# Performance work log

Hardware: AMD Instinct MI355X
Metric: run time of the kernel (lower is better)

## Reference

```python
import jax, jax.numpy as jnp
import numpy as np

B, S = 128, 32
V, E, H, L = 32000, 512, 1024, 2


def setup_inputs() -> dict:
    key = jax.random.key(0)
    ks = jax.random.split(key, 16)
    s = 0.02  # weight scale
    inp = {
        "x": jax.random.randint(ks[0], (B, S), 0, V),
        "encoder_output": jax.random.normal(ks[1], (S, B, H), jnp.float32),  # unused by module
        "encoder_hidden_state": jax.random.normal(ks[2], (L, B, H), jnp.float32),
        "emb": jax.random.normal(ks[3], (V, E), jnp.float32) * s,
        "w_ih0": jax.random.normal(ks[4], (3 * H, E), jnp.float32) * s,
        "w_hh0": jax.random.normal(ks[5], (3 * H, H), jnp.float32) * s,
        "b_ih0": jax.random.normal(ks[6], (3 * H,), jnp.float32) * s,
        "b_hh0": jax.random.normal(ks[7], (3 * H,), jnp.float32) * s,
        "w_ih1": jax.random.normal(ks[8], (3 * H, H), jnp.float32) * s,
        "w_hh1": jax.random.normal(ks[9], (3 * H, H), jnp.float32) * s,
        "b_ih1": jax.random.normal(ks[10], (3 * H,), jnp.float32) * s,
        "b_hh1": jax.random.normal(ks[11], (3 * H,), jnp.float32) * s,
        "w_dec": jax.random.normal(ks[12], (V, H), jnp.float32) * s,
        "b_dec": jax.random.normal(ks[13], (V,), jnp.float32) * s,
        "max_seq_length": S,
    }
    return inp


def _gru_cell(h, xt, w_ih, w_hh, b_ih, b_hh):
    # PyTorch GRU gate math
    gi = xt @ w_ih.T + b_ih  # [B, 3H]
    gh = h @ w_hh.T + b_hh   # [B, 3H]
    ir, iz, inn = jnp.split(gi, 3, axis=-1)
    hr, hz, hn = jnp.split(gh, 3, axis=-1)
    r = jax.nn.sigmoid(ir + hr)
    z = jax.nn.sigmoid(iz + hz)
    n = jnp.tanh(inn + r * hn)
    return (1.0 - z) * n + z * h


def reference(x, encoder_output, encoder_hidden_state, emb,
              w_ih0, w_hh0, b_ih0, b_hh0,
              w_ih1, w_hh1, b_ih1, b_hh1,
              w_dec, b_dec, max_seq_length):
    # teaching_rate = 0.0 -> pure teacher forcing; dropout p=0.0 -> identity.
    # Step 0 consumes SOS token (id 1, from torch.ones().long()); steps 1..T-1 consume x[:, i].
    Bsz = x.shape[0]
    sos = jnp.ones((Bsz, 1), jnp.int32)
    toks = jnp.concatenate([sos, x[:, 1:max_seq_length].astype(jnp.int32)], axis=1)  # [B, T]
    xs = emb[toks].transpose(1, 0, 2)  # [T, B, E] (seq-first, matching permute(1,0,2))

    def step(carry, xt):
        h0, h1 = carry
        h0 = _gru_cell(h0, xt, w_ih0, w_hh0, b_ih0, b_hh0)
        h1 = _gru_cell(h1, h0, w_ih1, w_hh1, b_ih1, b_hh1)
        return (h0, h1), h1

    init = (encoder_hidden_state[0], encoder_hidden_state[1])
    _, ys = jax.lax.scan(step, init, xs)  # ys: [T, B, H]
    logits = jnp.einsum('tbh,vh->tbv', ys, w_dec) + b_dec  # [T, B, V]
    return logits
```

## Files before the change

kernel.cpp:

```cpp
#include <hip/hip_runtime.h>
#include <hip/hip_bf16.h>
#include <stdint.h>

#define T_SEQ 32
#define BATCH 128
#define EMB   512
#define HID   1024
#define VOC   32000
#define G3    (3 * HID)
#define MROWS (T_SEQ * BATCH)
#define BHID  (BATCH * HID)

typedef __bf16 bf16_t;
typedef __bf16 bf16x8 __attribute__((ext_vector_type(8)));
typedef __bf16 bf16x4 __attribute__((ext_vector_type(4)));
typedef float  f32x4  __attribute__((ext_vector_type(4)));

#define MFMA(a, b, c) __builtin_amdgcn_mfma_f32_16x16x32_bf16((a), (b), (c), 0, 0, 0)

__global__ void f32_to_bf16_kernel(const float* __restrict__ in,
                                   bf16_t* __restrict__ out, int n) {
    int i = (blockIdx.x * blockDim.x + threadIdx.x) * 4;
    if (i + 3 < n) {
        float4 v = *(const float4*)(in + i);
        out[i + 0] = (bf16_t)v.x;
        out[i + 1] = (bf16_t)v.y;
        out[i + 2] = (bf16_t)v.z;
        out[i + 3] = (bf16_t)v.w;
    } else {
        for (; i < n; ++i) out[i] = (bf16_t)in[i];
    }
}

__global__ void embed_kernel(const int* __restrict__ x,
                             const float* __restrict__ emb,
                             bf16_t* __restrict__ X) {
    int m = blockIdx.x;
    int t = m >> 7, b = m & 127;
    int tok = (t == 0) ? 1 : x[b * T_SEQ + t];
    const float* src = emb + (size_t)tok * EMB;
    bf16_t* dst = X + (size_t)m * EMB;
    int c = threadIdx.x * 4;
    float4 v = *(const float4*)(src + c);
    dst[c + 0] = (bf16_t)v.x;
    dst[c + 1] = (bf16_t)v.y;
    dst[c + 2] = (bf16_t)v.z;
    dst[c + 3] = (bf16_t)v.w;
}

#define GLOAD_LDS16(g, l)                                                    \
    __builtin_amdgcn_global_load_lds(                                        \
        (const __attribute__((address_space(1))) void*)(g),                  \
        (__attribute__((address_space(3))) void*)(l), 16, 0, 0)

template <int BIAS>
__global__ __launch_bounds__(256) void gemm_bf16_kernel(
    const bf16_t* __restrict__ A, const bf16_t* __restrict__ B,
    const float* __restrict__ bias, float* __restrict__ C,
    int M, int N, int K) {
    __shared__ __align__(16) bf16_t As[128 * 32];
    __shared__ __align__(16) bf16_t Bs[128 * 32];

    const int nbm = gridDim.y, nbn = gridDim.x;
    const int nwg = nbm * nbn;
    int lin = blockIdx.y * nbn + blockIdx.x;
    if ((nwg & 7) == 0) {
        int xcd = lin & 7, idx = lin >> 3;
        lin = xcd * (nwg >> 3) + idx;
    }
    const int bm = (lin % nbm) * 128;
    const int bn = (lin / nbm) * 128;

    const int tid  = threadIdx.x;
    const int lane = tid & 63;
    const int w    = tid >> 6;
    const int wr   = w >> 1, wc = w & 1;

    f32x4 acc[4][4] = {};

    const int lrow = tid >> 2;
    const int lcol = (tid & 3) * 8;
    const bf16_t* ag = A + (size_t)(bm + lrow) * K + lcol;
    const bf16_t* bg = B + (size_t)(bn + lrow) * K + lcol;
    bf16_t* asl0 = As + lrow * 32 + lcol;
    bf16_t* asl1 = As + (lrow + 64) * 32 + lcol;
    bf16_t* bsl0 = Bs + lrow * 32 + lcol;
    bf16_t* bsl1 = Bs + (lrow + 64) * 32 + lcol;

    const int r16 = lane & 15;
    const int kh  = (lane >> 4) * 8;

    for (int k0 = 0; k0 < K; k0 += 32) {
        GLOAD_LDS16(ag + k0, asl0);
        GLOAD_LDS16(ag + (size_t)64 * K + k0, asl1);
        GLOAD_LDS16(bg + k0, bsl0);
        GLOAD_LDS16(bg + (size_t)64 * K + k0, bsl1);
        __syncthreads();

        bf16x8 af[4], bf[4];
#pragma unroll
        for (int mi = 0; mi < 4; ++mi)
            af[mi] = *(const bf16x8*)(As + (wr * 64 + mi * 16 + r16) * 32 + kh);
#pragma unroll
        for (int ni = 0; ni < 4; ++ni)
            bf[ni] = *(const bf16x8*)(Bs + (wc * 64 + ni * 16 + r16) * 32 + kh);
#pragma unroll
        for (int mi = 0; mi < 4; ++mi)
#pragma unroll
            for (int ni = 0; ni < 4; ++ni)
                acc[mi][ni] = MFMA(af[mi], bf[ni], acc[mi][ni]);
        __syncthreads();
    }

#pragma unroll
    for (int mi = 0; mi < 4; ++mi) {
        const int row0 = bm + wr * 64 + mi * 16 + (lane >> 4) * 4;
#pragma unroll
        for (int ni = 0; ni < 4; ++ni) {
            const int col = bn + wc * 64 + ni * 16 + r16;
            float bv = 0.f;
            if (BIAS) bv = bias[col];
#pragma unroll
            for (int r = 0; r < 4; ++r)
                C[(size_t)(row0 + r) * N + col] = acc[mi][ni][r] + bv;
        }
    }
}

template <int BIAS>
__global__ __launch_bounds__(512, 1) void gemm256_bf16_kernel(
    const bf16_t* __restrict__ A, const bf16_t* __restrict__ B,
    const float* __restrict__ bias, float* __restrict__ C,
    int M, int N, int K) {
    __shared__ __align__(16) bf16_t lds[2 * 2 * 16384];

    const int NT = K >> 6;
    const int nbm = gridDim.y, nbn = gridDim.x;
    const int nwg = nbm * nbn;
    int lin = blockIdx.y * nbn + blockIdx.x;
    {
        int q = nwg >> 3, r = nwg & 7, x = lin & 7, i = lin >> 3;
        lin = (x < r ? x * (q + 1) : r * (q + 1) + (x - r) * q) + i;
    }
    const int bm = (lin % nbm) * 256;
    const int bn = (lin / nbm) * 256;

    const int tid = threadIdx.x, lane = tid & 63;
    const int w = tid >> 6, wm = w >> 2, wn = w & 3;
    const int r16 = lane & 15, sl = lane >> 4, r7 = r16 & 7;

    const int srow  = tid >> 3;
    const int sslot = (tid & 7) ^ (srow & 7);
    const bf16_t* agS = A + (size_t)(bm + srow) * K + sslot * 8;
    const bf16_t* bgS = B + (size_t)(bn + srow) * K + sslot * 8;

    const int colk0 = ((0 + sl) ^ r7) * 8;
    const int colk1 = ((4 + sl) ^ r7) * 8;
    const int arow = (wm * 128 + r16) * 64;
    const int brow = (wn * 64 + r16) * 64;

    f32x4 acc[8][4] = {};
    bf16x8 af[4][2], bf[4][2];

#pragma unroll
    for (int l = 0; l < 4; ++l)
        GLOAD_LDS16(agS + (size_t)(l * 64) * K, lds + l * 4096 + tid * 8);
#pragma unroll
    for (int l = 0; l < 4; ++l)
        GLOAD_LDS16(bgS + (size_t)(l * 64) * K, lds + 16384 + l * 4096 + tid * 8);
#pragma unroll
    for (int l = 0; l < 4; ++l)
        GLOAD_LDS16(agS + (size_t)(l * 64) * K + 64,
                    lds + 32768 + l * 4096 + tid * 8);
#pragma unroll
    for (int l = 0; l < 4; ++l)
        GLOAD_LDS16(bgS + (size_t)(l * 64) * K + 64,
                    lds + 49152 + l * 4096 + tid * 8);
    asm volatile("s_waitcnt vmcnt(8)" ::: "memory");
    __builtin_amdgcn_sched_barrier(0);
    __builtin_amdgcn_s_barrier();

#pragma unroll 1
    for (int kt = 0; kt < NT; ++kt) {
        const int cur = kt & 1;
        const bf16_t* Ab = lds + cur * 32768;
        const bf16_t* Bb = Ab + 16384;
        bf16_t* Sb = lds + cur * 32768;
        const bool st = (kt + 2 < NT);
        const size_t kof = (size_t)(kt + 2) * 64;

#pragma unroll
        for (int fr = 0; fr < 4; ++fr) {
            af[fr][0] = *(const bf16x8*)(Ab + arow + fr * 1024 + colk0);
            af[fr][1] = *(const bf16x8*)(Ab + arow + fr * 1024 + colk1);
        }
#pragma unroll
        for (int nf = 0; nf < 2; ++nf) {
            bf[nf][0] = *(const bf16x8*)(Bb + brow + nf * 1024 + colk0);
            bf[nf][1] = *(const bf16x8*)(Bb + brow + nf * 1024 + colk1);
        }
        __builtin_amdgcn_sched_barrier(0);
        __builtin_amdgcn_s_barrier();
        asm volatile("s_waitcnt lgkmcnt(0)" ::: "memory");
        __builtin_amdgcn_sched_barrier(0);
        __builtin_amdgcn_s_setprio(1);
#pragma unroll
        for (int fr = 0; fr < 4; ++fr)
#pragma unroll
            for (int nf = 0; nf < 2; ++nf) {
                acc[fr][nf] = MFMA(af[fr][0], bf[nf][0], acc[fr][nf]);
                acc[fr][nf] = MFMA(af[fr][1], bf[nf][1], acc[fr][nf]);
            }
        __builtin_amdgcn_s_setprio(0);
        __builtin_amdgcn_sched_barrier(0);
        __builtin_amdgcn_s_barrier();

#pragma unroll
        for (int nf = 2; nf < 4; ++nf) {
            bf[nf][0] = *(const bf16x8*)(Bb + brow + nf * 1024 + colk0);
            bf[nf][1] = *(const bf16x8*)(Bb + brow + nf * 1024 + colk1);
        }
        __builtin_amdgcn_sched_barrier(0);
        if (st) {
            GLOAD_LDS16(agS + kof, Sb + tid * 8);
            GLOAD_LDS16(agS + (size_t)128 * K + kof, Sb + 8192 + tid * 8);
        }
        __builtin_amdgcn_s_barrier();
        asm volatile("s_waitcnt lgkmcnt(0)" ::: "memory");
        __builtin_amdgcn_sched_barrier(0);
        __builtin_amdgcn_s_setprio(1);
#pragma unroll
        for (int fr = 0; fr < 4; ++fr)
#pragma unroll
            for (int nf = 2; nf < 4; ++nf) {
                acc[fr][nf] = MFMA(af[fr][0], bf[nf][0], acc[fr][nf]);
                acc[fr][nf] = MFMA(af[fr][1], bf[nf][1], acc[fr][nf]);
            }
        __builtin_amdgcn_s_setprio(0);
        __builtin_amdgcn_sched_barrier(0);
        __builtin_amdgcn_s_barrier();

#pragma unroll
        for (int fr = 0; fr < 4; ++fr) {
            af[fr][0] = *(const bf16x8*)(Ab + arow + (fr + 4) * 1024 + colk0);
            af[fr][1] = *(const bf16x8*)(Ab + arow + (fr + 4) * 1024 + colk1);
        }
        __builtin_amdgcn_sched_barrier(0);
        if (st) {
#pragma unroll
            for (int l = 0; l < 4; ++l)
                GLOAD_LDS16(bgS + (size_t)(l * 64) * K + kof,
                            Sb + 16384 + l * 4096 + tid * 8);
        }
        __builtin_amdgcn_s_barrier();
        asm volatile("s_waitcnt lgkmcnt(0)" ::: "memory");
        __builtin_amdgcn_sched_barrier(0);
        __builtin_amdgcn_s_setprio(1);
#pragma unroll
        for (int fr = 0; fr < 4; ++fr)
#pragma unroll
            for (int nf = 0; nf < 2; ++nf) {
                acc[fr + 4][nf] = MFMA(af[fr][0], bf[nf][0], acc[fr + 4][nf]);
                acc[fr + 4][nf] = MFMA(af[fr][1], bf[nf][1], acc[fr + 4][nf]);
            }
        __builtin_amdgcn_s_setprio(0);
        __builtin_amdgcn_sched_barrier(0);
        __builtin_amdgcn_s_barrier();

        if (st) {
            GLOAD_LDS16(agS + (size_t)64 * K + kof, Sb + 4096 + tid * 8);
            GLOAD_LDS16(agS + (size_t)192 * K + kof, Sb + 12288 + tid * 8);
        }
        if (kt + 2 < NT) {
            asm volatile("s_waitcnt vmcnt(8)" ::: "memory");
        } else if (kt + 1 < NT) {
            asm volatile("s_waitcnt vmcnt(0)" ::: "memory");
        }
        __builtin_amdgcn_sched_barrier(0);
        __builtin_amdgcn_s_setprio(1);
#pragma unroll
        for (int fr = 0; fr < 4; ++fr)
#pragma unroll
            for (int nf = 2; nf < 4; ++nf) {
                acc[fr + 4][nf] = MFMA(af[fr][0], bf[nf][0], acc[fr + 4][nf]);
                acc[fr + 4][nf] = MFMA(af[fr][1], bf[nf][1], acc[fr + 4][nf]);
            }
        __builtin_amdgcn_s_setprio(0);
        __builtin_amdgcn_sched_barrier(0);
        __builtin_amdgcn_s_barrier();
    }

#pragma unroll
    for (int fr = 0; fr < 8; ++fr) {
        const int row0 = bm + wm * 128 + fr * 16 + sl * 4;
#pragma unroll
        for (int nf = 0; nf < 4; ++nf) {
            const int col = bn + wn * 64 + nf * 16 + r16;
            float bv = 0.f;
            if (BIAS) bv = bias[col];
#pragma unroll
            for (int r = 0; r < 4; ++r)
                __builtin_nontemporal_store(
                    acc[fr][nf][r] + bv, &C[(size_t)(row0 + r) * N + col]);
        }
    }
}

union U64cast  { bf16x4 v; unsigned long long u; };
union U128cast { f32x4 v; unsigned long long u[2]; };

__global__ __launch_bounds__(256, 1) void fused_scan_kernel(
    const bf16_t* __restrict__ h0ib, const bf16_t* __restrict__ h1ib,
    const float* __restrict__ enc_hid,
    const bf16_t* __restrict__ whh0, const bf16_t* __restrict__ wih1,
    const bf16_t* __restrict__ whh1,
    const float* __restrict__ bhh0, const float* __restrict__ bih1,
    const float* __restrict__ bhh1,
    float* __restrict__ Gi, bf16_t* __restrict__ H0b,
    bf16_t* __restrict__ H1b, unsigned* __restrict__ flags) {
    __shared__ __align__(16) float Sg[4][3][128][16];

    const int tid  = threadIdx.x;
    const int lane = tid & 63;
    const int w    = tid >> 6;
    const int role = blockIdx.x >> 6;
    const int cb   = blockIdx.x & 63;
    const int c0   = cb * 16;
    const int r16  = lane & 15;
    const int kq   = (lane >> 4) * 8;

    const bf16_t* whh = role == 0 ? whh0 : (role == 1 ? wih1 : whh1);
    const float*  bia = role == 0 ? bhh0 : (role == 1 ? bih1 : bhh1);

    bf16x8 wf[3][8];
#pragma unroll
    for (int g = 0; g < 3; ++g)
#pragma unroll
        for (int kf = 0; kf < 8; ++kf)
            wf[g][kf] = *(const bf16x8*)(
                whh + (size_t)(g * HID + c0 + r16) * HID + w * 256 + kf * 32 + kq);

    const int cg   = tid & 3;
    const int rloc = tid >> 2;
    const int ce   = c0 + cg * 4;

    float bh[3][4];
#pragma unroll
    for (int g = 0; g < 3; ++g)
#pragma unroll
        for (int j = 0; j < 4; ++j) bh[g][j] = bia[g * HID + ce + j];

    float hp[2][4];
    if (role != 1) {
        const float* h0f = enc_hid + (role == 2 ? BHID : 0);
#pragma unroll
        for (int i = 0; i < 2; ++i)
#pragma unroll
            for (int j = 0; j < 4; ++j)
                hp[i][j] = h0f[(size_t)(rloc + i * 64) * HID + ce + j];
    }

    for (int t = 0; t < T_SEQ; ++t) {
        if (role == 0) {
            if (t && tid < 64)
                while (__hip_atomic_load(&flags[tid], __ATOMIC_RELAXED,
                                         __HIP_MEMORY_SCOPE_SYSTEM) <
                       (unsigned)t)
                    __builtin_amdgcn_s_sleep(1);
        } else if (role == 1) {
            if (tid < 64)
                while (__hip_atomic_load(&flags[tid], __ATOMIC_RELAXED,
                                         __HIP_MEMORY_SCOPE_SYSTEM) <
                       (unsigned)(t + 1))
                    __builtin_amdgcn_s_sleep(1);
        } else {
            if (tid < 64) {
                while (__hip_atomic_load(&flags[64 + tid], __ATOMIC_RELAXED,
                                         __HIP_MEMORY_SCOPE_SYSTEM) <
                       (unsigned)(t + 1))
                    __builtin_amdgcn_s_sleep(1);
            } else if (tid < 128 && t) {
                while (__hip_atomic_load(&flags[128 + tid - 64],
                                         __ATOMIC_RELAXED,
                                         __HIP_MEMORY_SCOPE_SYSTEM) <
                       (unsigned)t)
                    __builtin_amdgcn_s_sleep(1);
            }
        }
        __syncthreads();

        f32x4 gi[2][3];
        if (role == 0) {
#pragma unroll
            for (int i = 0; i < 2; ++i) {
                const size_t gb =
                    ((size_t)t * BATCH + rloc + i * 64) * G3 + ce;
                gi[i][0] = *(const f32x4*)(Gi + gb);
                gi[i][1] = *(const f32x4*)(Gi + gb + HID);
                gi[i][2] = *(const f32x4*)(Gi + gb + 2 * HID);
            }
        } else if (role == 2) {
#pragma unroll
            for (int i = 0; i < 2; ++i) {
                const size_t gb =
                    ((size_t)t * BATCH + rloc + i * 64) * G3 + ce;
#pragma unroll
                for (int g = 0; g < 3; ++g) {
                    U128cast u;
                    const unsigned long long* p =
                        (const unsigned long long*)(Gi + gb + g * HID);
                    u.u[0] = __hip_atomic_load(p, __ATOMIC_RELAXED,
                                               __HIP_MEMORY_SCOPE_SYSTEM);
                    u.u[1] = __hip_atomic_load(p + 1, __ATOMIC_RELAXED,
                                               __HIP_MEMORY_SCOPE_SYSTEM);
                    gi[i][g] = u.v;
                }
            }
        }

        const bf16_t* hb =
            role == 0 ? (t ? H0b + (size_t)(t - 1) * BHID : h0ib)
          : role == 1 ? (H0b + (size_t)t * BHID)
                      : (t ? H1b + (size_t)(t - 1) * BHID : h1ib);

        f32x4 acc[3][8] = {};
        bf16x8 af[4][8];
#define LD_GROUP(buf, kf)                                                    \
    {                                                                        \
        const int kbase = w * 256 + (kf) * 32 + kq;                          \
        _Pragma("unroll") for (int rf = 0; rf < 8; ++rf)                     \
            af[buf][rf] =                                                    \
                *(const bf16x8*)(hb + (size_t)(rf * 16 + r16) * HID + kbase); \
    }
        LD_GROUP(0, 0)
        LD_GROUP(1, 1)
        LD_GROUP(2, 2)
#pragma unroll
        for (int kf = 0; kf < 8; ++kf) {
            if (kf + 3 < 8) LD_GROUP((kf + 3) & 3, kf + 3)
#pragma unroll
            for (int rf = 0; rf < 8; ++rf) {
                acc[0][rf] = MFMA(af[kf & 3][rf], wf[0][kf], acc[0][rf]);
                acc[1][rf] = MFMA(af[kf & 3][rf], wf[1][kf], acc[1][rf]);
                acc[2][rf] = MFMA(af[kf & 3][rf], wf[2][kf], acc[2][rf]);
            }
        }
#undef LD_GROUP

#pragma unroll
        for (int g = 0; g < 3; ++g)
#pragma unroll
            for (int rf = 0; rf < 8; ++rf)
#pragma unroll
                for (int r = 0; r < 4; ++r)
                    Sg[w][g][rf * 16 + (lane >> 4) * 4 + r][r16] = acc[g][rf][r];
        __syncthreads();

#pragma unroll
        for (int i = 0; i < 2; ++i) {
            const int row = rloc + i * 64;
            f32x4 gr = *(const f32x4*)&Sg[0][0][row][cg * 4];
            f32x4 gz = *(const f32x4*)&Sg[0][1][row][cg * 4];
            f32x4 gn = *(const f32x4*)&Sg[0][2][row][cg * 4];
#pragma unroll
            for (int ks = 1; ks < 4; ++ks) {
                gr += *(const f32x4*)&Sg[ks][0][row][cg * 4];
                gz += *(const f32x4*)&Sg[ks][1][row][cg * 4];
                gn += *(const f32x4*)&Sg[ks][2][row][cg * 4];
            }
            if (role == 1) {
                const size_t gb =
                    ((size_t)t * BATCH + row) * G3 + ce;
                U128cast s0, s1, s2;
#pragma unroll
                for (int j = 0; j < 4; ++j) {
                    s0.v[j] = gr[j] + bh[0][j];
                    s1.v[j] = gz[j] + bh[1][j];
                    s2.v[j] = gn[j] + bh[2][j];
                }
                unsigned long long* p0 = (unsigned long long*)(Gi + gb);
                unsigned long long* p1 = (unsigned long long*)(Gi + gb + HID);
                unsigned long long* p2 = (unsigned long long*)(Gi + gb + 2 * HID);
                __hip_atomic_store(p0, s0.u[0], __ATOMIC_RELAXED, __HIP_MEMORY_SCOPE_SYSTEM);
                __hip_atomic_store(p0 + 1, s0.u[1], __ATOMIC_RELAXED, __HIP_MEMORY_SCOPE_SYSTEM);
                __hip_atomic_store(p1, s1.u[0], __ATOMIC_RELAXED, __HIP_MEMORY_SCOPE_SYSTEM);
                __hip_atomic_store(p1 + 1, s1.u[1], __ATOMIC_RELAXED, __HIP_MEMORY_SCOPE_SYSTEM);
                __hip_atomic_store(p2, s2.u[0], __ATOMIC_RELAXED, __HIP_MEMORY_SCOPE_SYSTEM);
                __hip_atomic_store(p2 + 1, s2.u[1], __ATOMIC_RELAXED, __HIP_MEMORY_SCOPE_SYSTEM);
            } else {
                U64cast hb4;
#pragma unroll
                for (int j = 0; j < 4; ++j) {
                    float rr = 1.f / (1.f + __expf(-(gi[i][0][j] + gr[j] + bh[0][j])));
                    float zz = 1.f / (1.f + __expf(-(gi[i][1][j] + gz[j] + bh[1][j])));
                    float nn = tanhf(gi[i][2][j] + rr * (gn[j] + bh[2][j]));
                    float h  = (1.f - zz) * nn + zz * hp[i][j];
                    hp[i][j] = h;
                    hb4.v[j] = (bf16_t)h;
                }
                bf16_t* dst = (role == 0 ? H0b : H1b) +
                              (size_t)t * BHID + (size_t)row * HID + ce;
                __hip_atomic_store((unsigned long long*)dst, hb4.u,
                                   __ATOMIC_RELAXED, __HIP_MEMORY_SCOPE_SYSTEM);
            }
        }

        __syncthreads();
        if (tid == 0)
            __hip_atomic_store(&flags[role * 64 + cb], (unsigned)(t + 1),
                               __ATOMIC_RELAXED, __HIP_MEMORY_SCOPE_SYSTEM);
    }
}

extern "C" void kernel_launch(void* const* d_in, const int* in_sizes, int n_in,
                              void* d_out, int out_size, void* d_ws, size_t ws_size,
                              hipStream_t stream) {
    const int*   x        = (const int*)d_in[0];
    const float* enc_hid  = (const float*)d_in[2];
    const float* emb      = (const float*)d_in[3];
    const float* w_ih0    = (const float*)d_in[4];
    const float* w_hh0    = (const float*)d_in[5];
    const float* b_ih0    = (const float*)d_in[6];
    const float* b_hh0    = (const float*)d_in[7];
    const float* w_ih1    = (const float*)d_in[8];
    const float* w_hh1    = (const float*)d_in[9];
    const float* b_ih1    = (const float*)d_in[10];
    const float* b_hh1    = (const float*)d_in[11];
    const float* w_dec    = (const float*)d_in[12];
    const float* b_dec    = (const float*)d_in[13];
    float* out = (float*)d_out;

    char* ws = (char*)d_ws;
    size_t off = 0;
    auto alloc = [&](size_t bytes) {
        void* p = ws + off;
        off += (bytes + 255) & ~(size_t)255;
        return p;
    };
    unsigned* flags  = (unsigned*)alloc(1024);
    bf16_t* Xb     = (bf16_t*)alloc((size_t)MROWS * EMB * 2);
    bf16_t* Wih0b  = (bf16_t*)alloc((size_t)G3 * EMB * 2);
    bf16_t* Whh0b  = (bf16_t*)alloc((size_t)G3 * HID * 2);
    bf16_t* Wih1b  = (bf16_t*)alloc((size_t)G3 * HID * 2);
    bf16_t* Whh1b  = (bf16_t*)alloc((size_t)G3 * HID * 2);
    bf16_t* Wdecb  = (bf16_t*)alloc((size_t)VOC * HID * 2);
    bf16_t* h0ib   = (bf16_t*)alloc((size_t)BATCH * HID * 2);
    bf16_t* h1ib   = (bf16_t*)alloc((size_t)BATCH * HID * 2);
    float*  Gi     = (float*)alloc((size_t)MROWS * G3 * 4);
    bf16_t* H0b    = (bf16_t*)alloc((size_t)MROWS * HID * 2);
    bf16_t* H1b    = (bf16_t*)alloc((size_t)MROWS * HID * 2);

    hipMemsetAsync(flags, 0, 1024, stream);

    auto cvt = [&](const float* src, bf16_t* dst, int n) {
        int blocks = (n + 1023) / 1024;
        f32_to_bf16_kernel<<<blocks, 256, 0, stream>>>(src, dst, n);
    };

    cvt(w_ih0, Wih0b, G3 * EMB);
    cvt(w_hh0, Whh0b, G3 * HID);
    cvt(w_ih1, Wih1b, G3 * HID);
    cvt(w_hh1, Whh1b, G3 * HID);
    cvt(w_dec, Wdecb, VOC * HID);
    cvt(enc_hid, h0ib, BATCH * HID);
    cvt(enc_hid + BATCH * HID, h1ib, BATCH * HID);

    embed_kernel<<<MROWS, 128, 0, stream>>>(x, emb, Xb);

    gemm_bf16_kernel<1><<<dim3(G3 / 128, MROWS / 128), 256, 0, stream>>>(
        Xb, Wih0b, b_ih0, Gi, MROWS, G3, EMB);

    fused_scan_kernel<<<192, 256, 0, stream>>>(
        h0ib, h1ib, enc_hid, Whh0b, Wih1b, Whh1b,
        b_hh0, b_ih1, b_hh1, Gi, H0b, H1b, flags);

    gemm256_bf16_kernel<1><<<dim3(VOC / 256, MROWS / 256), 512, 0, stream>>>(
        H1b, Wdecb, b_dec, out, MROWS, VOC, HID);
}
```

Baseline: 935.2 us.

## Narrow scan flag waits to per-wave dependencies and defer role-2 Gi wait

Each wave now spins only on the 16 producer-block flags that cover its own K-slice of the hidden state, and the block-wide barrier before the matmul is removed, so waves can start their MFMA work as soon as their own inputs are ready. Role 2 (layer-1 hidden recurrence) now runs its matmul before waiting for the role-1 input-gate results, and checks only the single flag for its own column block. This overlaps the layer-1 input projection with the layer-1 recurrent projection and is meant to shorten the critical path of each timestep. It depends on relaxed system-scope atomics giving enough ordering without a workgroup barrier, which carries some memory-visibility risk.

```diff
diff --git a/kernel.cpp b/kernel.cpp
--- a/kernel.cpp
+++ b/kernel.cpp
@@ -309,6 +309,13 @@
 union U64cast  { bf16x4 v; unsigned long long u; };
 union U128cast { f32x4 v; unsigned long long u[2]; };
 
+__device__ __forceinline__ unsigned flag_ld(const unsigned* p) {
+    return __hip_atomic_load(p, __ATOMIC_RELAXED, __HIP_MEMORY_SCOPE_SYSTEM);
+}
+__device__ __forceinline__ void flag_st(unsigned* p, unsigned v) {
+    __hip_atomic_store(p, v, __ATOMIC_RELAXED, __HIP_MEMORY_SCOPE_SYSTEM);
+}
+
 __global__ __launch_bounds__(256, 1) void fused_scan_kernel(
     const bf16_t* __restrict__ h0ib, const bf16_t* __restrict__ h1ib,
     const float* __restrict__ enc_hid,
@@ -328,6 +335,7 @@
     const int c0   = cb * 16;
     const int r16  = lane & 15;
     const int kq   = (lane >> 4) * 8;
+    const int pf   = w * 16 + (lane & 15);
 
     const bf16_t* whh = role == 0 ? whh0 : (role == 1 ? wih1 : whh1);
     const float*  bia = role == 0 ? bhh0 : (role == 1 ? bih1 : bhh1);
@@ -362,32 +370,17 @@
 
     for (int t = 0; t < T_SEQ; ++t) {
         if (role == 0) {
-            if (t && tid < 64)
-                while (__hip_atomic_load(&flags[tid], __ATOMIC_RELAXED,
-                                         __HIP_MEMORY_SCOPE_SYSTEM) <
-                       (unsigned)t)
+            if (t)
+                while (flag_ld(&flags[pf]) < (unsigned)t)
                     __builtin_amdgcn_s_sleep(1);
         } else if (role == 1) {
-            if (tid < 64)
-                while (__hip_atomic_load(&flags[tid], __ATOMIC_RELAXED,
-                                         __HIP_MEMORY_SCOPE_SYSTEM) <
-                       (unsigned)(t + 1))
+            while (flag_ld(&flags[pf]) < (unsigned)(t + 1))
+                __builtin_amdgcn_s_sleep(1);
+        } else {
+            if (t)
+                while (flag_ld(&flags[128 + pf]) < (unsigned)t)
                     __builtin_amdgcn_s_sleep(1);
-        } else {
-            if (tid < 64) {
-                while (__hip_atomic_load(&flags[64 + tid], __ATOMIC_RELAXED,
-                                         __HIP_MEMORY_SCOPE_SYSTEM) <
-                       (unsigned)(t + 1))
-                    __builtin_amdgcn_s_sleep(1);
-            } else if (tid < 128 && t) {
-                while (__hip_atomic_load(&flags[128 + tid - 64],
-                                         __ATOMIC_RELAXED,
-                                         __HIP_MEMORY_SCOPE_SYSTEM) <
-                       (unsigned)t)
-                    __builtin_amdgcn_s_sleep(1);
-            }
-        }
-        __syncthreads();
+        }
 
         f32x4 gi[2][3];
         if (role == 0) {
@@ -399,7 +392,49 @@
                 gi[i][1] = *(const f32x4*)(Gi + gb + HID);
                 gi[i][2] = *(const f32x4*)(Gi + gb + 2 * HID);
             }
-        } else if (role == 2) {
+        }
+
+        const bf16_t* hb =
+            role == 0 ? (t ? H0b + (size_t)(t - 1) * BHID : h0ib)
+          : role == 1 ? (H0b + (size_t)t * BHID)
+                      : (t ? H1b + (size_t)(t - 1) * BHID : h1ib);
+
+        f32x4 acc[3][8] = {};
+        bf16x8 af[4][8];
+#define LD_GROUP(buf, kf)                                                    \
+    {                                                                        \
+        const int kbase = w * 256 + (kf) * 32 + kq;                          \
+        _Pragma("unroll") for (int rf = 0; rf < 8; ++rf)                     \
+            af[buf][rf] =                                                    \
+                *(const bf16x8*)(hb + (size_t)(rf * 16 + r16) * HID + kbase); \
+    }
+        LD_GROUP(0, 0)
+        LD_GROUP(1, 1)
+        LD_GROUP(2, 2)
+#pragma unroll
+        for (int kf = 0; kf < 8; ++kf) {
+            if (kf + 3 < 8) LD_GROUP((kf + 3) & 3, kf + 3)
+#pragma unroll
+            for (int rf = 0; rf < 8; ++rf) {
+                acc[0][rf] = MFMA(af[kf & 3][rf], wf[0][kf], acc[0][rf]);
+                acc[1][rf] = MFMA(af[kf & 3][rf], wf[1][kf], acc[1][rf]);
+                acc[2][rf] = MFMA(af[kf & 3][rf], wf[2][kf], acc[2][rf]);
+            }
+        }
+#undef LD_GROUP
+
+#pragma unroll
+        for (int g = 0; g < 3; ++g)
+#pragma unroll
+            for (int rf = 0; rf < 8; ++rf)
+#pragma unroll
+                for (int r = 0; r < 4; ++r)
+                    Sg[w][g][rf * 16 + (lane >> 4) * 4 + r][r16] = acc[g][rf][r];
+        __syncthreads();
+
+        if (role == 2) {
+            while (flag_ld(&flags[64 + cb]) < (unsigned)(t + 1))
+                __builtin_amdgcn_s_sleep(1);
 #pragma unroll
             for (int i = 0; i < 2; ++i) {
                 const size_t gb =
@@ -417,44 +452,6 @@
                 }
             }
         }
-
-        const bf16_t* hb =
-            role == 0 ? (t ? H0b + (size_t)(t - 1) * BHID : h0ib)
-          : role == 1 ? (H0b + (size_t)t * BHID)
-                      : (t ? H1b + (size_t)(t - 1) * BHID : h1ib);
-
-        f32x4 acc[3][8] = {};
-        bf16x8 af[4][8];
-#define LD_GROUP(buf, kf)                                                    \
-    {                                                                        \
-        const int kbase = w * 256 + (kf) * 32 + kq;                          \
-        _Pragma("unroll") for (int rf = 0; rf < 8; ++rf)                     \
-            af[buf][rf] =                                                    \
-                *(const bf16x8*)(hb + (size_t)(rf * 16 + r16) * HID + kbase); \
-    }
-        LD_GROUP(0, 0)
-        LD_GROUP(1, 1)
-        LD_GROUP(2, 2)
-#pragma unroll
-        for (int kf = 0; kf < 8; ++kf) {
-            if (kf + 3 < 8) LD_GROUP((kf + 3) & 3, kf + 3)
-#pragma unroll
-            for (int rf = 0; rf < 8; ++rf) {
-                acc[0][rf] = MFMA(af[kf & 3][rf], wf[0][kf], acc[0][rf]);
-                acc[1][rf] = MFMA(af[kf & 3][rf], wf[1][kf], acc[1][rf]);
-                acc[2][rf] = MFMA(af[kf & 3][rf], wf[2][kf], acc[2][rf]);
-            }
-        }
-#undef LD_GROUP
-
-#pragma unroll
-        for (int g = 0; g < 3; ++g)
-#pragma unroll
-            for (int rf = 0; rf < 8; ++rf)
-#pragma unroll
-                for (int r = 0; r < 4; ++r)
-                    Sg[w][g][rf * 16 + (lane >> 4) * 4 + r][r16] = acc[g][rf][r];
-        __syncthreads();
 
 #pragma unroll
         for (int i = 0; i < 2; ++i) {
@@ -507,8 +504,7 @@
 
         __syncthreads();
         if (tid == 0)
-            __hip_atomic_store(&flags[role * 64 + cb], (unsigned)(t + 1),
-                               __ATOMIC_RELAXED, __HIP_MEMORY_SCOPE_SYSTEM);
+            flag_st(&flags[role * 64 + cb], (unsigned)(t + 1));
     }
 }
 
```

New measurement: 966.6 us. 3.4% more time.
